# Performance work log

Hardware: AMD Instinct MI355X
Metric: run time of the kernel (lower is better)

The kernel has to match this reference:

```python
import jax, jax.numpy as jnp
import numpy as np

B, N, H = 8, 128, 768      # batch, words, BERT hidden
HID, L = 384, 100          # MLP hidden, label_num


def setup_inputs() -> dict:
    key = jax.random.key(0)
    k0, k1, k2 = jax.random.split(key, 3)
    s = 0.02
    return {
        "repr_w": jax.random.normal(k0, (B, N, H), jnp.float32),
        "W1": jax.random.normal(k1, (2 * H, HID), jnp.float32) * s,
        "b1": jnp.zeros((HID,), jnp.float32),
        "W2": jax.random.normal(k2, (HID, L), jnp.float32) * s,
        "b2": jnp.zeros((L,), jnp.float32),
    }


def reference(repr_w, W1, b1, W2, b2):
    # Original: table[b,i,j] = concat(repr_w[b,j] (row_h), repr_w[b,i] (column_h))
    # then MLP: relu(table @ W1 + b1) @ W2 + b2  (dropout inactive in eval).
    # Decompose the concat-GEMM: concat(r_j, r_i) @ W1 == r_j @ W1[:H] + r_i @ W1[H:].
    W1_row, W1_col = W1[:H], W1[H:]
    p = jnp.einsum('bnh,hd->bnd', repr_w, W1_row)  # contribution indexed by j
    q = jnp.einsum('bnh,hd->bnd', repr_w, W1_col)  # contribution indexed by i
    h = jax.nn.relu(p[:, None, :, :] + q[:, :, None, :] + b1)  # [B,N,N,HID]
    return jnp.einsum('bijd,dl->bijl', h, W2) + b2              # [B,N,N,L]
```

## Files before the change

### kernel.cpp

```cpp
#include <hip/hip_runtime.h>
#include <hip/hip_bf16.h>

#define B_   8
#define N_   128
#define H_   768
#define HID_ 384
#define L_   100

typedef float f32x4 __attribute__((ext_vector_type(4)));
typedef short s16x8 __attribute__((ext_vector_type(8)));

__device__ __forceinline__ short f2bf(float f) {
    __hip_bfloat16 h = __float2bfloat16(f);
    return __builtin_bit_cast(short, h);
}

__device__ __forceinline__ void gl_lds16(const void* g, void* l) {
    __builtin_amdgcn_global_load_lds(
        (const __attribute__((address_space(1))) unsigned int*)g,
        (__attribute__((address_space(3))) unsigned int*)l, 16, 0, 0);
}

__global__ void prep_w1f(const float* __restrict__ W1, short* __restrict__ W1f) {
    int tid = blockIdx.x * 256 + threadIdx.x;
    if (tid >= 48 * 24 * 64) return;
    int lane = tid & 63;
    int kk   = (tid >> 6) % 24;
    int ct   = tid / (24 * 64);
    int c    = ct * 16 + (lane & 15);
    int k0   = kk * 32 + ((lane >> 4) << 3);
    short v[8];
#pragma unroll
    for (int e = 0; e < 8; ++e) {
        int k = k0 + e;
        float f = (c < HID_) ? W1[(size_t)k * HID_ + c]
                             : W1[(size_t)(H_ + k) * HID_ + (c - HID_)];
        v[e] = f2bf(f);
    }
    ((s16x8*)W1f)[tid] = *(const s16x8*)v;
}

__global__ void prep_w2f(const float* __restrict__ W2, short* __restrict__ W2f) {
    int tid = blockIdx.x * 256 + threadIdx.x;
    if (tid >= 12 * 7 * 64) return;
    int lane = tid & 63;
    int t    = (tid >> 6) % 7;
    int kk   = tid / (7 * 64);
    int c    = t * 16 + (lane & 15);
    int k0   = kk * 32 + ((lane >> 4) << 3);
    short v[8];
#pragma unroll
    for (int e = 0; e < 8; ++e) {
        float f = (c < L_) ? W2[(size_t)(k0 + e) * L_ + c] : 0.0f;
        v[e] = f2bf(f);
    }
    ((s16x8*)W2f)[tid] = *(const s16x8*)v;
}

__global__ __launch_bounds__(256) void pq_gemm(
    const float* __restrict__ repr, const short* __restrict__ W1f,
    const float* __restrict__ b1,
    float* __restrict__ Pt, float* __restrict__ Q)
{
    __shared__ float atile[192 * 16 * 4];
    const int rt   = blockIdx.x / 12;
    const int cg   = blockIdx.x % 12;
    const int w    = threadIdx.x >> 6;
    const int lane = threadIdx.x & 63;
    const int l15  = lane & 15;
    const int g    = lane >> 4;
    const int ct   = cg * 4 + w;
    const int row_g0 = rt * 16;

#pragma unroll
    for (int c = 0; c < 12; ++c) {
        int call = w * 12 + c;
        const float* src = repr + (size_t)(row_g0 + (lane & 15)) * H_
                         + (call * 4 + (lane >> 4)) * 4;
        gl_lds16(src, (char*)atile + call * 1024);
    }
    __syncthreads();

    f32x4 acc;
    acc[0] = 0.f; acc[1] = 0.f; acc[2] = 0.f; acc[3] = 0.f;
    const s16x8* bbase = (const s16x8*)W1f + (size_t)(ct * 24) * 64 + lane;

#pragma unroll 4
    for (int kk = 0; kk < 24; ++kk) {
        const int u0 = kk * 8 + g * 2;
        float a[8];
        *(float4*)&a[0] = *(const float4*)&atile[(u0 * 16 + l15) * 4];
        *(float4*)&a[4] = *(const float4*)&atile[((u0 + 1) * 16 + l15) * 4];
        s16x8 af;
#pragma unroll
        for (int e = 0; e < 8; ++e) af[e] = f2bf(a[e]);
        s16x8 bf = bbase[(size_t)kk * 64];
        acc = __builtin_amdgcn_mfma_f32_16x16x32_bf16(af, bf, acc, 0, 0, 0);
    }

    const int b = rt >> 3;
    const int c = ct * 16 + l15;
#pragma unroll
    for (int r = 0; r < 4; ++r) {
        int brow = (rt & 7) * 16 + g * 4 + r;
        float v = acc[r];
        if (c < HID_) {
            int slice = c >> 5, un = (c & 31) >> 2, e4 = c & 3;
            Pt[((((size_t)b * 12 + slice) * 8 + un) * 128 + brow) * 4 + e4] = v + b1[c];
        } else {
            Q[(size_t)(b * N_ + brow) * HID_ + (c - HID_)] = v;
        }
    }
}

__global__ __launch_bounds__(256) void fused_out(
    const float* __restrict__ Pt, const float* __restrict__ Q,
    const short* __restrict__ W2f, const float* __restrict__ b2,
    float* __restrict__ out)
{
    __shared__ float pbuf[2][8 * 64 * 4];
    __shared__ float qlds[2 * HID_];

    const int blk   = blockIdx.x;
    const int b     = blk >> 7;
    const int ipair = (blk >> 1) & 63;
    const int jh    = blk & 1;
    const int i0    = ipair * 2;
    const int w     = threadIdx.x >> 6;
    const int lane  = threadIdx.x & 63;
    const int l15   = lane & 15;
    const int g     = lane >> 4;
    const int j0    = jh * 64 + w * 16;
    const int jl0   = w * 16;

    if (w == 3) {
        const float* qsrc = Q + (size_t)(b * N_ + i0) * HID_;
#pragma unroll
        for (int c2 = 0; c2 < 3; ++c2)
            gl_lds16(qsrc + c2 * 256 + lane * 4, (char*)qlds + c2 * 1024);
    }
#pragma unroll
    for (int h2 = 0; h2 < 2; ++h2) {
        int u = w * 2 + h2;
        const float* src = Pt + ((((size_t)b * 12 + 0) * 8 + u) * 128 + jh * 64 + lane) * 4;
        gl_lds16(src, (char*)&pbuf[0][0] + u * 1024);
    }
    __syncthreads();

    f32x4 acc[2][7];
#pragma unroll
    for (int ii = 0; ii < 2; ++ii)
#pragma unroll
        for (int t = 0; t < 7; ++t) {
            acc[ii][t][0] = 0.f; acc[ii][t][1] = 0.f;
            acc[ii][t][2] = 0.f; acc[ii][t][3] = 0.f;
        }

#pragma unroll
    for (int kk = 0; kk < 12; ++kk) {
        const int cur = kk & 1;
        if (kk < 11) {
#pragma unroll
            for (int h2 = 0; h2 < 2; ++h2) {
                int u = w * 2 + h2;
                const float* src = Pt + ((((size_t)b * 12 + (kk + 1)) * 8 + u) * 128
                                         + jh * 64 + lane) * 4;
                gl_lds16(src, (char*)&pbuf[cur ^ 1][0] + u * 1024);
            }
        }

        float p[8], q0v[8], q1v[8];
        *(float4*)&p[0]   = *(const float4*)&pbuf[cur][((g * 2 + 0) * 64 + jl0 + l15) * 4];
        *(float4*)&p[4]   = *(const float4*)&pbuf[cur][((g * 2 + 1) * 64 + jl0 + l15) * 4];
        *(float4*)&q0v[0] = *(const float4*)&qlds[0 * HID_ + kk * 32 + g * 8];
        *(float4*)&q0v[4] = *(const float4*)&qlds[0 * HID_ + kk * 32 + g * 8 + 4];
        *(float4*)&q1v[0] = *(const float4*)&qlds[1 * HID_ + kk * 32 + g * 8];
        *(float4*)&q1v[4] = *(const float4*)&qlds[1 * HID_ + kk * 32 + g * 8 + 4];

        s16x8 af0, af1;
#pragma unroll
        for (int e = 0; e < 8; ++e) {
            af0[e] = f2bf(fmaxf(p[e] + q0v[e], 0.f));
            af1[e] = f2bf(fmaxf(p[e] + q1v[e], 0.f));
        }

        const s16x8* bfp = (const s16x8*)W2f + (size_t)(kk * 7) * 64 + lane;
#pragma unroll
        for (int t = 0; t < 7; ++t) {
            s16x8 bf = bfp[(size_t)t * 64];
            acc[0][t] = __builtin_amdgcn_mfma_f32_16x16x32_bf16(af0, bf, acc[0][t], 0, 0, 0);
            acc[1][t] = __builtin_amdgcn_mfma_f32_16x16x32_bf16(af1, bf, acc[1][t], 0, 0, 0);
        }
        __syncthreads();
    }

    float bias[7];
#pragma unroll
    for (int t = 0; t < 7; ++t) {
        int l = t * 16 + l15;
        bias[t] = (l < L_) ? b2[l] : 0.f;
    }

#pragma unroll
    for (int ii = 0; ii < 2; ++ii) {
        const size_t obase = (size_t)(b * N_ + (i0 + ii)) * N_ * L_;
#pragma unroll
        for (int r = 0; r < 4; ++r) {
            int j = j0 + g * 4 + r;
            float* op = out + obase + (size_t)j * L_;
#pragma unroll
            for (int t = 0; t < 7; ++t) {
                int l = t * 16 + l15;
                if (l < L_) op[l] = acc[ii][t][r] + bias[t];
            }
        }
    }
}

extern "C" void kernel_launch(void* const* d_in, const int* in_sizes, int n_in,
                              void* d_out, int out_size, void* d_ws, size_t ws_size,
                              hipStream_t stream)
{
    const float* repr = (const float*)d_in[0];
    const float* W1   = (const float*)d_in[1];
    const float* b1   = (const float*)d_in[2];
    const float* W2   = (const float*)d_in[3];
    const float* b2   = (const float*)d_in[4];
    float* out = (float*)d_out;

    char* ws = (char*)d_ws;
    float* Pt  = (float*)(ws);
    float* Qm  = (float*)(ws + 1572864);
    short* W1f = (short*)(ws + 3145728);
    short* W2f = (short*)(ws + 4325376);

    hipLaunchKernelGGL(prep_w1f,  dim3(288),  dim3(256), 0, stream, W1, W1f);
    hipLaunchKernelGGL(prep_w2f,  dim3(21),   dim3(256), 0, stream, W2, W2f);
    hipLaunchKernelGGL(pq_gemm,   dim3(768),  dim3(256), 0, stream, repr, W1f, b1, Pt, Qm);
    hipLaunchKernelGGL(fused_out, dim3(1024), dim3(256), 0, stream, Pt, Qm, W2f, b2, out);
}
```

Baseline: 123.1 us.

## Widen fused_out blocks to full j range, stage W2 in LDS, coalesce output stores

```diff
diff --git a/kernel.cpp b/kernel.cpp
--- a/kernel.cpp
+++ b/kernel.cpp
@@ -113,37 +113,37 @@
     }
 }
 
-__global__ __launch_bounds__(256) void fused_out(
+__global__ __launch_bounds__(512, 4) void fused_out(
     const float* __restrict__ Pt, const float* __restrict__ Q,
     const short* __restrict__ W2f, const float* __restrict__ b2,
     float* __restrict__ out)
 {
-    __shared__ float pbuf[2][8 * 64 * 4];
-    __shared__ float qlds[2 * HID_];
-
-    const int blk   = blockIdx.x;
-    const int b     = blk >> 7;
-    const int ipair = (blk >> 1) & 63;
-    const int jh    = blk & 1;
-    const int i0    = ipair * 2;
-    const int w     = threadIdx.x >> 6;
-    const int lane  = threadIdx.x & 63;
-    const int l15   = lane & 15;
-    const int g     = lane >> 4;
-    const int j0    = jh * 64 + w * 16;
-    const int jl0   = w * 16;
-
-    if (w == 3) {
-        const float* qsrc = Q + (size_t)(b * N_ + i0) * HID_;
+    __shared__ __align__(16) char smem[58368];
+    char* pbufB  = smem;
+    char* w2bufB = smem + 32768;
+    char* qldsB  = smem + 47104;
+    float* storeF = (float*)smem;
+
+    const int blk  = blockIdx.x;
+    const int b    = blk >> 6;
+    const int i0   = (blk & 63) << 1;
+    const int w    = threadIdx.x >> 6;
+    const int lane = threadIdx.x & 63;
+    const int l15  = lane & 15;
+    const int g    = lane >> 4;
+
+    const char* ptb = (const char*)Pt + (size_t)b * 12 * 16384;
+    const char* w2g = (const char*)W2f;
+
+    gl_lds16(ptb + w * 2048 + lane * 16,        pbufB + w * 2048);
+    gl_lds16(ptb + w * 2048 + 1024 + lane * 16, pbufB + w * 2048 + 1024);
+    if (w < 7)
+        gl_lds16(w2g + w * 1024 + lane * 16, w2bufB + w * 1024);
+    if (w == 7) {
+        const char* qsrc = (const char*)(Q + (size_t)(b * N_ + i0) * HID_);
 #pragma unroll
         for (int c2 = 0; c2 < 3; ++c2)
-            gl_lds16(qsrc + c2 * 256 + lane * 4, (char*)qlds + c2 * 1024);
-    }
-#pragma unroll
-    for (int h2 = 0; h2 < 2; ++h2) {
-        int u = w * 2 + h2;
-        const float* src = Pt + ((((size_t)b * 12 + 0) * 8 + u) * 128 + jh * 64 + lane) * 4;
-        gl_lds16(src, (char*)&pbuf[0][0] + u * 1024);
+            gl_lds16(qsrc + c2 * 1024 + lane * 16, qldsB + c2 * 1024);
     }
     __syncthreads();
 
@@ -156,26 +156,29 @@
             acc[ii][t][2] = 0.f; acc[ii][t][3] = 0.f;
         }
 
+    const float* qF = (const float*)qldsB;
+
 #pragma unroll
     for (int kk = 0; kk < 12; ++kk) {
         const int cur = kk & 1;
         if (kk < 11) {
-#pragma unroll
-            for (int h2 = 0; h2 < 2; ++h2) {
-                int u = w * 2 + h2;
-                const float* src = Pt + ((((size_t)b * 12 + (kk + 1)) * 8 + u) * 128
-                                         + jh * 64 + lane) * 4;
-                gl_lds16(src, (char*)&pbuf[cur ^ 1][0] + u * 1024);
-            }
-        }
-
+            const char* src = ptb + (size_t)(kk + 1) * 16384 + w * 2048;
+            char* dst = pbufB + (cur ^ 1) * 16384 + w * 2048;
+            gl_lds16(src + lane * 16,        dst);
+            gl_lds16(src + 1024 + lane * 16, dst + 1024);
+            if (w < 7)
+                gl_lds16(w2g + (size_t)((kk + 1) * 7 + w) * 1024 + lane * 16,
+                         w2bufB + (cur ^ 1) * 7168 + w * 1024);
+        }
+
+        const float* pF = (const float*)(pbufB + cur * 16384);
         float p[8], q0v[8], q1v[8];
-        *(float4*)&p[0]   = *(const float4*)&pbuf[cur][((g * 2 + 0) * 64 + jl0 + l15) * 4];
-        *(float4*)&p[4]   = *(const float4*)&pbuf[cur][((g * 2 + 1) * 64 + jl0 + l15) * 4];
-        *(float4*)&q0v[0] = *(const float4*)&qlds[0 * HID_ + kk * 32 + g * 8];
-        *(float4*)&q0v[4] = *(const float4*)&qlds[0 * HID_ + kk * 32 + g * 8 + 4];
-        *(float4*)&q1v[0] = *(const float4*)&qlds[1 * HID_ + kk * 32 + g * 8];
-        *(float4*)&q1v[4] = *(const float4*)&qlds[1 * HID_ + kk * 32 + g * 8 + 4];
+        *(float4*)&p[0] = *(const float4*)&pF[((g * 2 + 0) * 128 + w * 16 + l15) * 4];
+        *(float4*)&p[4] = *(const float4*)&pF[((g * 2 + 1) * 128 + w * 16 + l15) * 4];
+        *(float4*)&q0v[0] = *(const float4*)&qF[0 * HID_ + kk * 32 + g * 8];
+        *(float4*)&q0v[4] = *(const float4*)&qF[0 * HID_ + kk * 32 + g * 8 + 4];
+        *(float4*)&q1v[0] = *(const float4*)&qF[1 * HID_ + kk * 32 + g * 8];
+        *(float4*)&q1v[4] = *(const float4*)&qF[1 * HID_ + kk * 32 + g * 8 + 4];
 
         s16x8 af0, af1;
 #pragma unroll
@@ -184,7 +187,7 @@
             af1[e] = f2bf(fmaxf(p[e] + q1v[e], 0.f));
         }
 
-        const s16x8* bfp = (const s16x8*)W2f + (size_t)(kk * 7) * 64 + lane;
+        const s16x8* bfp = (const s16x8*)(w2bufB + cur * 7168) + lane;
 #pragma unroll
         for (int t = 0; t < 7; ++t) {
             s16x8 bf = bfp[(size_t)t * 64];
@@ -201,17 +204,22 @@
         bias[t] = (l < L_) ? b2[l] : 0.f;
     }
 
+    __syncthreads();
+    float* srow = storeF + w * (16 * 114);
+
 #pragma unroll
     for (int ii = 0; ii < 2; ++ii) {
+#pragma unroll
+        for (int t = 0; t < 7; ++t)
+#pragma unroll
+            for (int r = 0; r < 4; ++r)
+                srow[(g * 4 + r) * 114 + t * 16 + l15] = acc[ii][t][r] + bias[t];
         const size_t obase = (size_t)(b * N_ + (i0 + ii)) * N_ * L_;
 #pragma unroll
-        for (int r = 0; r < 4; ++r) {
-            int j = j0 + g * 4 + r;
-            float* op = out + obase + (size_t)j * L_;
-#pragma unroll
-            for (int t = 0; t < 7; ++t) {
-                int l = t * 16 + l15;
-                if (l < L_) op[l] = acc[ii][t][r] + bias[t];
+        for (int row = 0; row < 16; ++row) {
+            if (lane < 50) {
+                float2 v = *(const float2*)&srow[row * 114 + lane * 2];
+                *(float2*)(out + obase + (size_t)(w * 16 + row) * L_ + lane * 2) = v;
             }
         }
     }
@@ -234,8 +242,8 @@
     short* W1f = (short*)(ws + 3145728);
     short* W2f = (short*)(ws + 4325376);
 
-    hipLaunchKernelGGL(prep_w1f,  dim3(288),  dim3(256), 0, stream, W1, W1f);
-    hipLaunchKernelGGL(prep_w2f,  dim3(21),   dim3(256), 0, stream, W2, W2f);
-    hipLaunchKernelGGL(pq_gemm,   dim3(768),  dim3(256), 0, stream, repr, W1f, b1, Pt, Qm);
-    hipLaunchKernelGGL(fused_out, dim3(1024), dim3(256), 0, stream, Pt, Qm, W2f, b2, out);
-}
+    hipLaunchKernelGGL(prep_w1f,  dim3(288), dim3(256), 0, stream, W1, W1f);
+    hipLaunchKernelGGL(prep_w2f,  dim3(21),  dim3(256), 0, stream, W2, W2f);
+    hipLaunchKernelGGL(pq_gemm,   dim3(768), dim3(256), 0, stream, repr, W1f, b1, Pt, Qm);
+    hipLaunchKernelGGL(fused_out, dim3(512), dim3(512), 0, stream, Pt, Qm, W2f, b2, out);
+}
```

Result: faster. 108.1 us (-12.1%).
